# Optimization experiments

Measured on AMD Instinct MI355X. Metric: run time of the kernel, lower is better.

The kernel has to match this reference:

```python
import jax, jax.numpy as jnp
import numpy as np

B, L, H = 64, 512, 512          # batch, max_len, hidden_size (code requires H == L)
ITEM = 50001                    # item_num + 1
TEMP = 0.2                      # gumbel-sigmoid temperature
EPS = 1e-20


def setup_inputs() -> dict:
    key = jax.random.key(0)
    ks = jax.random.split(key, 16)
    lin = lambda k: jax.random.normal(k, (L, L), jnp.float32) * (1.0 / np.sqrt(L))
    U = jax.random.uniform(ks[13], (L, H), jnp.float32)
    gumbel = -jnp.log(-jnp.log(U + EPS) + EPS)
    return {
        "positives": jax.random.randint(ks[0], (B, L), 0, ITEM),
        "mask": jax.random.randint(ks[1], (B, L), 0, 2).astype(jnp.int32),
        "item_emb": jax.random.normal(ks[2], (ITEM, H), jnp.float32) * 0.02,
        "pos_emb": jax.random.normal(ks[3], (L, H), jnp.float32) * 0.02,
        "Wz": lin(ks[4]),
        "Wv": lin(ks[5]),
        "Wq": lin(ks[6]),
        "Wk": lin(ks[7]),
        "gamma_q": jax.random.normal(ks[8], (L,), jnp.float32) * 0.02,
        "beta_q": jnp.zeros((L,), jnp.float32),
        "gamma_k": jax.random.normal(ks[9], (L,), jnp.float32) * 0.02,
        "beta_k": jnp.zeros((L,), jnp.float32),
        "sparse_w": jax.random.uniform(ks[10], (L, H), jnp.float32, 0.2, 0.8),
        "gumbel": gumbel,
    }


def reference(positives, mask, item_emb, pos_emb, Wz, Wv, Wq, Wk,
              gamma_q, beta_q, gamma_k, beta_k, sparse_w, gumbel):
    # ---- merge_attn_masks: True = masked ----
    pad = ~(mask.astype(bool))[:, None, :]                 # [B,1,L]
    future = jnp.triu(jnp.ones((L, L), bool), k=1)         # strictly upper
    merged = pad | future[None]                            # [B,L,L]
    attn_mask = (~jnp.eye(L, dtype=bool))[None] & merged   # keep diagonal unmasked

    # ---- embeddings ----
    x = item_emb[positives] + pos_emb[None]                # [B,L,H]

    # ---- GAU-style projections (Linear acts on last dim, y = x @ W^T) ----
    z = jax.nn.silu(x @ Wz.T)                              # [B,L,H]
    v = jax.nn.silu(x @ Wv.T)                              # [B,L,H]
    q = (z @ Wq.T) * gamma_q + beta_q                      # OffsetScale head 0
    k = (z @ Wk.T) * gamma_k + beta_k

    # ---- relu^2 attention with bool mask added then zeroed ----
    m = attn_mask.astype(q.dtype)
    a = jnp.einsum('bld,bmd->blm', q, k) + m               # torch adds bool as 0/1
    a = a * (1.0 - m)                                      # a * ~attn_mask

    # ---- gumbel-sigmoid sparse mask (broadcast [L,L] over batch) ----
    smask = jax.nn.sigmoid((jnp.log(sparse_w / (1.0 - sparse_w)) + gumbel) / TEMP)
    a = smask[None] * a

    a = jnp.square(jax.nn.relu(a)) / (L * H)
    return a @ v                                           # [B,L,H]
```

## Files before the change

kernel.cpp:

```cpp
#include <hip/hip_runtime.h>
#include <hip/hip_fp16.h>
#include <math.h>

typedef _Float16 f16;
typedef unsigned int u32;
typedef _Float16 f16x8 __attribute__((ext_vector_type(8)));
typedef _Float16 f16x4 __attribute__((ext_vector_type(4)));
typedef float    f32x4 __attribute__((ext_vector_type(4)));

constexpr int LEN  = 512;
constexpr int HID  = 512;
constexpr int BATCH = 64;

#define BM 128
#define BN 128
#define BK 64

__device__ __forceinline__ void gload16(const f16* g, f16* l) {
    __builtin_amdgcn_global_load_lds((const __attribute__((address_space(1))) u32*)g,
                                     (__attribute__((address_space(3))) u32*)l,
                                     16, 0, 0);
}

__device__ __forceinline__ void gemm_core(const f16* __restrict__ A, int lda,
                                          const f16* __restrict__ Bm, int ldb,
                                          int ksteps,
                                          f16* ldsA, f16* ldsB,
                                          f32x4 acc[4][4])
{
    const int tid  = threadIdx.x;
    const int lane = tid & 63;
    const int wv   = tid >> 6;
    const int wr   = wv >> 1, wc = wv & 1;
    const int mf   = lane & 15;
    const int kf   = (lane >> 4) * 8;

    for (int r = 0; r < 4; ++r)
        for (int c = 0; c < 4; ++c)
            acc[r][c] = (f32x4){0.f, 0.f, 0.f, 0.f};

    for (int kt = 0; kt < ksteps; ++kt) {
        const int k0 = kt * BK;
        #pragma unroll
        for (int j = 0; j < 4; ++j) {
            const int cb  = j * 256 + wv * 64;
            const int c   = cb + lane;
            const int row = c >> 3;
            const int col = (c & 7) << 3;
            gload16(A  + (size_t)row * lda + (k0 + col), ldsA + cb * 8);
            gload16(Bm + (size_t)row * ldb + (k0 + col), ldsB + cb * 8);
        }
        __syncthreads();
        #pragma unroll
        for (int kk = 0; kk < BK; kk += 32) {
            f16x8 af[4], bf[4];
            #pragma unroll
            for (int r = 0; r < 4; ++r) {
                af[r] = *(const f16x8*)(ldsA + (wr * 64 + r * 16 + mf) * BK + kk + kf);
                bf[r] = *(const f16x8*)(ldsB + (wc * 64 + r * 16 + mf) * BK + kk + kf);
            }
            #pragma unroll
            for (int r = 0; r < 4; ++r)
                #pragma unroll
                for (int c = 0; c < 4; ++c)
                    acc[r][c] = __builtin_amdgcn_mfma_f32_16x16x32_f16(af[r], bf[c], acc[r][c], 0, 0, 0);
        }
        __syncthreads();
    }
}

#define EPILOGUE_IDX() \
    const int lane = threadIdx.x & 63, wv_ = threadIdx.x >> 6;   \
    const int wr = wv_ >> 1, wc = wv_ & 1;                       \
    const int c0 = lane & 15, r0 = (lane >> 4) * 4;

__device__ __forceinline__ void store_tile_f16(f16* lds, const f16 vals[4][4][4],
                                               f16* __restrict__ gout, int ldo)
{
    const int tid = threadIdx.x;
    EPILOGUE_IDX();
    #pragma unroll
    for (int r = 0; r < 4; ++r)
        #pragma unroll
        for (int c = 0; c < 4; ++c)
            #pragma unroll
            for (int i = 0; i < 4; ++i) {
                const int lr = wr * 64 + r * 16 + r0 + i;
                const int lc = wc * 64 + c * 16 + c0;
                lds[lr * 128 + lc] = vals[r][c][i];
            }
    __syncthreads();
    #pragma unroll
    for (int ph = 0; ph < 8; ++ph) {
        const int row = ph * 16 + (tid >> 4);
        const int col = (tid & 15) * 8;
        *(f16x8*)(gout + (size_t)row * ldo + col) = *(const f16x8*)(lds + row * 128 + col);
    }
}

__device__ __forceinline__ float silu_f(float v) {
    return v * __builtin_amdgcn_rcpf(1.f + __expf(-v));
}

__global__ __launch_bounds__(256) void k_zv(const f16* __restrict__ x,
                                            const f16* __restrict__ Wzh,
                                            const f16* __restrict__ Wvh,
                                            f16* __restrict__ z,
                                            f16* __restrict__ vt)
{
    const int bid = blockIdx.x;
    const int s = (bid & 7) + 8 * (bid >> 6);
    const int i = (bid >> 3) & 7;
    __shared__ f16 lds[(BM + BN) * BK];
    f32x4 acc[4][4];
    f16 vals[4][4][4];
    if (i < 4) {
        gemm_core(x + (size_t)s * BM * HID, HID,
                  Wzh + (size_t)i * BN * HID, HID,
                  HID / BK, lds, lds + BM * BK, acc);
        #pragma unroll
        for (int r = 0; r < 4; ++r)
            #pragma unroll
            for (int c = 0; c < 4; ++c)
                #pragma unroll
                for (int q = 0; q < 4; ++q)
                    vals[r][c][q] = (f16)silu_f(acc[r][c][q]);
        store_tile_f16(lds, vals, z + (size_t)s * BM * HID + i * BN, HID);
    } else {
        const int ht = i - 4, b = s >> 2, mt = s & 3;
        gemm_core(Wvh + (size_t)ht * BM * HID, HID,
                  x + ((size_t)b * LEN + mt * BN) * HID, HID,
                  HID / BK, lds, lds + BM * BK, acc);
        #pragma unroll
        for (int r = 0; r < 4; ++r)
            #pragma unroll
            for (int c = 0; c < 4; ++c)
                #pragma unroll
                for (int q = 0; q < 4; ++q)
                    vals[r][c][q] = (f16)silu_f(acc[r][c][q]);
        store_tile_f16(lds, vals,
                       vt + (size_t)b * LEN * HID + (size_t)ht * BM * LEN + mt * BN, LEN);
    }
}

__global__ __launch_bounds__(256) void k_qkp(const f16* __restrict__ z,
                                             const f16* __restrict__ Wqh,
                                             const f16* __restrict__ Wkh,
                                             const float* __restrict__ gq,
                                             const float* __restrict__ bq,
                                             const float* __restrict__ gk,
                                             const float* __restrict__ bk,
                                             f16* __restrict__ qh,
                                             f16* __restrict__ kh)
{
    const int bid = blockIdx.x;
    const int s = (bid & 7) + 8 * (bid >> 6);
    const int i = (bid >> 3) & 7;
    const bool isq = i < 4;
    const int tn = isq ? i : i - 4;
    const f16* W = isq ? Wqh : Wkh;
    const float* g = isq ? gq : gk;
    const float* be = isq ? bq : bk;
    f16* out = isq ? qh : kh;
    __shared__ f16 lds[(BM + BN) * BK];
    f32x4 acc[4][4];
    gemm_core(z + (size_t)s * BM * HID, HID,
              W + (size_t)tn * BN * HID, HID,
              HID / BK, lds, lds + BM * BK, acc);
    f16 vals[4][4][4];
    {
        EPILOGUE_IDX();
        #pragma unroll
        for (int r = 0; r < 4; ++r)
            #pragma unroll
            for (int c = 0; c < 4; ++c) {
                const int gj = tn * BN + wc * 64 + c * 16 + c0;
                const float ga = g[gj], ba = be[gj];
                #pragma unroll
                for (int q = 0; q < 4; ++q)
                    vals[r][c][q] = (f16)((acc[r][c][q] * ga + ba) * 1024.f);
            }
    }
    store_tile_f16(lds, vals, out + (size_t)s * BM * HID + tn * BN, HID);
}

__constant__ int LT_TAB[10] = {0,1,1,2,2,2,3,3,3,3};
__constant__ int MT_TAB[10] = {0,0,1,0,1,2,0,1,2,3};

__global__ __launch_bounds__(256) void k_qk(const f16* __restrict__ q,
                                            const f16* __restrict__ kmat,
                                            const int* __restrict__ mask,
                                            const float* __restrict__ smask,
                                            f16* __restrict__ p)
{
    const int bid = blockIdx.x;
    const int t = (bid >> 3) % 10;
    const int b = (bid & 7) + 8 * (bid / 80);
    const int lt = LT_TAB[t], mt = MT_TAB[t];
    __shared__ f16 lds[(BM + BN) * BK];
    f32x4 acc[4][4];
    const size_t boff = (size_t)b * LEN * HID;
    gemm_core(q + boff + (size_t)lt * BM * HID, HID,
              kmat + boff + (size_t)mt * BN * HID, HID,
              HID / BK, lds, lds + BM * BK, acc);
    f16 vals[4][4][4];
    {
        EPILOGUE_IDX();
        #pragma unroll
        for (int r = 0; r < 4; ++r)
            #pragma unroll
            for (int c = 0; c < 4; ++c) {
                const int m = mt * BN + wc * 64 + c * 16 + c0;
                const int keepcol = mask[b * LEN + m];
                #pragma unroll
                for (int i = 0; i < 4; ++i) {
                    const int l = lt * BM + wr * 64 + r * 16 + r0 + i;
                    const bool keep = (l == m) || ((m <= l) && (keepcol != 0));
                    float v = keep ? acc[r][c][i] * smask[l * LEN + m] : 0.f;
                    v = fmaxf(v, 0.f);
                    vals[r][c][i] = (f16)(v * v);
                }
            }
    }
    store_tile_f16(lds, vals, p + (size_t)b * LEN * LEN + (size_t)lt * BM * LEN + mt * BN, LEN);
}

__global__ __launch_bounds__(256) void k_pv(const f16* __restrict__ p,
                                            const f16* __restrict__ vt,
                                            float* __restrict__ out)
{
    const int bid = blockIdx.x;
    const int inner = (bid >> 3) & 15;
    const int b = (bid & 7) + 8 * (bid >> 7);
    const int lt = 3 - (inner >> 2), ht = inner & 3;
    __shared__ f16 lds[(BM + BN) * BK];
    f32x4 acc[4][4];
    gemm_core(p + (size_t)b * LEN * LEN + (size_t)lt * BM * LEN, LEN,
              vt + (size_t)b * HID * LEN + (size_t)ht * BN * LEN, LEN,
              (lt + 1) * BM / BK, lds, lds + BM * BK, acc);
    EPILOGUE_IDX();
    const float SCALE = 3.4694469519536142e-18f;
    #pragma unroll
    for (int r = 0; r < 4; ++r)
        #pragma unroll
        for (int c = 0; c < 4; ++c) {
            const int h = ht * BN + wc * 64 + c * 16 + c0;
            #pragma unroll
            for (int i = 0; i < 4; ++i) {
                const int l = lt * BM + wr * 64 + r * 16 + r0 + i;
                out[(size_t)b * LEN * HID + (size_t)l * HID + h] = acc[r][c][i] * SCALE;
            }
        }
}

__global__ __launch_bounds__(256) void k_prep(const int* __restrict__ pos,
                                              const float* __restrict__ item_emb,
                                              const float* __restrict__ pos_emb,
                                              f16* __restrict__ x,
                                              const float* __restrict__ Wz,
                                              const float* __restrict__ Wv,
                                              const float* __restrict__ Wq,
                                              const float* __restrict__ Wk,
                                              f16* __restrict__ Wzh,
                                              f16* __restrict__ Wvh,
                                              f16* __restrict__ Wqh,
                                              f16* __restrict__ Wkh,
                                              const float* __restrict__ sw,
                                              const float* __restrict__ gum,
                                              float* __restrict__ smask)
{
    const int bid = blockIdx.x;
    const int tid = threadIdx.x;
    if (bid < 16384) {
        const int t = bid * 256 + tid;
        const int i = t >> 7;
        const int c = t & 127;
        const int l = i & (LEN - 1);
        const int item = pos[i];
        const float4 a  = ((const float4*)(item_emb + (size_t)item * HID))[c];
        const float4 b4 = ((const float4*)(pos_emb + (size_t)l * HID))[c];
        f16x4 o = { (f16)(a.x + b4.x), (f16)(a.y + b4.y),
                    (f16)(a.z + b4.z), (f16)(a.w + b4.w) };
        *(f16x4*)(x + (size_t)t * 4) = o;
    } else if (bid < 16384 + 1024) {
        const int r = bid - 16384;
        const int w = r >> 8;
        const float* s = (w == 0) ? Wz : (w == 1) ? Wv : (w == 2) ? Wq : Wk;
        f16* d = (w == 0) ? Wzh : (w == 1) ? Wvh : (w == 2) ? Wqh : Wkh;
        const int t = (r & 255) * 256 + tid;
        const float4 v = ((const float4*)s)[t];
        f16x4 o = { (f16)v.x, (f16)v.y, (f16)v.z, (f16)v.w };
        *(f16x4*)(d + (size_t)t * 4) = o;
    } else {
        const int t = (bid - 16384 - 1024) * 256 + tid;
        const float4 w4 = ((const float4*)sw)[t];
        const float4 g4 = ((const float4*)gum)[t];
        float4 o;
        o.x = __builtin_amdgcn_rcpf(1.f + __expf(-(__logf(w4.x / (1.f - w4.x)) + g4.x) * 5.f));
        o.y = __builtin_amdgcn_rcpf(1.f + __expf(-(__logf(w4.y / (1.f - w4.y)) + g4.y) * 5.f));
        o.z = __builtin_amdgcn_rcpf(1.f + __expf(-(__logf(w4.z / (1.f - w4.z)) + g4.z) * 5.f));
        o.w = __builtin_amdgcn_rcpf(1.f + __expf(-(__logf(w4.w / (1.f - w4.w)) + g4.w) * 5.f));
        ((float4*)smask)[t] = o;
    }
}

extern "C" void kernel_launch(void* const* d_in, const int* in_sizes, int n_in,
                              void* d_out, int out_size, void* d_ws, size_t ws_size,
                              hipStream_t stream)
{
    const int*   positives = (const int*)  d_in[0];
    const int*   mask      = (const int*)  d_in[1];
    const float* item_emb  = (const float*)d_in[2];
    const float* pos_emb   = (const float*)d_in[3];
    const float* Wz        = (const float*)d_in[4];
    const float* Wv        = (const float*)d_in[5];
    const float* Wq        = (const float*)d_in[6];
    const float* Wk        = (const float*)d_in[7];
    const float* gamma_q   = (const float*)d_in[8];
    const float* beta_q    = (const float*)d_in[9];
    const float* gamma_k   = (const float*)d_in[10];
    const float* beta_k    = (const float*)d_in[11];
    const float* sparse_w  = (const float*)d_in[12];
    const float* gumbel    = (const float*)d_in[13];
    float* out = (float*)d_out;

    char* ws = (char*)d_ws;
    const size_t BUFB = (size_t)BATCH * LEN * HID * sizeof(f16);
    f16* buf0 = (f16*)ws;
    f16* buf1 = (f16*)(ws + BUFB);
    f16* buf2 = (f16*)(ws + 2 * BUFB);
    f16* Wzh  = (f16*)(ws + 3 * BUFB);
    f16* Wvh  = Wzh + LEN * HID;
    f16* Wqh  = Wvh + LEN * HID;
    f16* Wkh  = Wqh + LEN * HID;
    float* smask = (float*)(Wkh + LEN * HID);
    f16* qh = (f16*)d_out;
    f16* kh = qh + (size_t)BATCH * LEN * HID;

    k_prep<<<16384 + 1024 + 256, 256, 0, stream>>>(
        positives, item_emb, pos_emb, buf0,
        Wz, Wv, Wq, Wk, Wzh, Wvh, Wqh, Wkh,
        sparse_w, gumbel, smask);

    k_zv<<<2048, 256, 0, stream>>>(buf0, Wzh, Wvh, buf1, buf2);

    k_qkp<<<2048, 256, 0, stream>>>(buf1, Wqh, Wkh,
                                    gamma_q, beta_q, gamma_k, beta_k, qh, kh);

    k_qk<<<640, 256, 0, stream>>>(qh, kh, mask, smask, buf0);

    k_pv<<<1024, 256, 0, stream>>>(buf0, buf2, out);
}
```

Before: 372.6 us.

## Replace projection GEMMs with 256x256 tiled, triple-buffered 8-wave kernels

The z/v and q/k projection kernels move from 128x128 tiles with 256 threads to 256x256 tiles with 512 threads (8 waves). Each wave computes a 128x64 sub-tile. K is consumed in 32-wide steps through a three-deep LDS ring filled by direct global-to-LDS loads with XOR-swizzled slots, and MFMA bursts are interleaved with staged loads under raised wave priority. The aim is more operand reuse per byte loaded and better overlap of memory with compute. In exchange each block uses about 136 KB of LDS, and the grid shrinks to 512 blocks, which lowers occupancy.

```diff
diff --git a/kernel.cpp b/kernel.cpp
--- a/kernel.cpp
+++ b/kernel.cpp
@@ -20,6 +20,200 @@
     __builtin_amdgcn_global_load_lds((const __attribute__((address_space(1))) u32*)g,
                                      (__attribute__((address_space(3))) u32*)l,
                                      16, 0, 0);
+}
+
+__device__ __forceinline__ float silu_f(float v) {
+    return v * __builtin_amdgcn_rcpf(1.f + __expf(-v));
+}
+
+#define LDSP 272
+
+__device__ __forceinline__ void stage_pass8(const f16* __restrict__ g, f16* l) {
+    const int tid = threadIdx.x;
+    const int row = tid >> 2;
+    const int sc  = (tid & 3) ^ (row & 3);
+    gload16(g + (size_t)row * HID + sc * 8, l + (tid >> 6) * 512);
+}
+
+__device__ __forceinline__ void stage_tile8(const f16* __restrict__ A,
+                                            const f16* __restrict__ B,
+                                            int kt, f16* buf) {
+    stage_pass8(A + kt * 32,             buf);
+    stage_pass8(A + kt * 32 + 128 * HID, buf + 4096);
+    stage_pass8(B + kt * 32,             buf + 8192);
+    stage_pass8(B + kt * 32 + 128 * HID, buf + 12288);
+}
+
+__device__ __forceinline__ void gemm8_core(const f16* __restrict__ A,
+                                           const f16* __restrict__ B,
+                                           f16* lds, f32x4 acc[8][4])
+{
+    const int tid  = threadIdx.x;
+    const int lane = tid & 63;
+    const int wv   = tid >> 6;
+    const int wr   = wv >> 2, wc = wv & 3;
+    const int mf   = lane & 15;
+    const int slot = ((lane >> 4) ^ (mf & 3)) * 8;
+    const int aoff = (wr * 128 + mf) * 32 + slot;
+    const int boff = (wc * 64  + mf) * 32 + slot + 8192;
+
+    #pragma unroll
+    for (int m = 0; m < 8; ++m)
+        #pragma unroll
+        for (int n = 0; n < 4; ++n)
+            acc[m][n] = (f32x4){0.f, 0.f, 0.f, 0.f};
+
+    stage_tile8(A, B, 0, lds);
+    stage_tile8(A, B, 1, lds + 16384);
+    asm volatile("s_waitcnt vmcnt(4)" ::: "memory");
+    __builtin_amdgcn_s_barrier();
+
+    f16x8 af[4], bf[4];
+    #pragma unroll
+    for (int kt = 0; kt < 16; ++kt) {
+        f16* buf  = lds + (kt % 3) * 16384;
+        f16* nbuf = lds + ((kt + 2) % 3) * 16384;
+        const bool st = (kt < 14);
+
+        #pragma unroll
+        for (int m = 0; m < 4; ++m) af[m] = *(const f16x8*)(buf + aoff + m * 512);
+        #pragma unroll
+        for (int n = 0; n < 4; ++n) bf[n] = *(const f16x8*)(buf + boff + n * 512);
+        if (st) {
+            stage_pass8(A + (kt + 2) * 32,             nbuf);
+            stage_pass8(A + (kt + 2) * 32 + 128 * HID, nbuf + 4096);
+        }
+        __builtin_amdgcn_s_barrier();
+        asm volatile("s_waitcnt lgkmcnt(0)" ::: "memory");
+        __builtin_amdgcn_sched_barrier(0);
+        __builtin_amdgcn_s_setprio(1);
+        #pragma unroll
+        for (int m = 0; m < 4; ++m)
+            #pragma unroll
+            for (int n = 0; n < 4; ++n)
+                acc[m][n] = __builtin_amdgcn_mfma_f32_16x16x32_f16(af[m], bf[n], acc[m][n], 0, 0, 0);
+        __builtin_amdgcn_s_setprio(0);
+        __builtin_amdgcn_s_barrier();
+
+        #pragma unroll
+        for (int m = 0; m < 4; ++m) af[m] = *(const f16x8*)(buf + aoff + (m + 4) * 512);
+        if (st) {
+            stage_pass8(B + (kt + 2) * 32,             nbuf + 8192);
+            stage_pass8(B + (kt + 2) * 32 + 128 * HID, nbuf + 12288);
+        }
+        __builtin_amdgcn_s_barrier();
+        asm volatile("s_waitcnt lgkmcnt(0)" ::: "memory");
+        __builtin_amdgcn_sched_barrier(0);
+        __builtin_amdgcn_s_setprio(1);
+        #pragma unroll
+        for (int m = 0; m < 4; ++m)
+            #pragma unroll
+            for (int n = 0; n < 4; ++n)
+                acc[m + 4][n] = __builtin_amdgcn_mfma_f32_16x16x32_f16(af[m], bf[n], acc[m + 4][n], 0, 0, 0);
+        __builtin_amdgcn_s_setprio(0);
+        if (kt < 14)       asm volatile("s_waitcnt vmcnt(4)" ::: "memory");
+        else if (kt == 14) asm volatile("s_waitcnt vmcnt(0)" ::: "memory");
+        __builtin_amdgcn_s_barrier();
+    }
+}
+
+__device__ __forceinline__ void store_tile8(const f16* lds, f16* __restrict__ gout, int ldo) {
+    const int tid = threadIdx.x;
+    #pragma unroll
+    for (int ph = 0; ph < 16; ++ph) {
+        const int r = ph * 16 + (tid >> 5);
+        const int c = (tid & 31) * 8;
+        *(f16x8*)(gout + (size_t)r * ldo + c) = *(const f16x8*)(lds + r * LDSP + c);
+    }
+}
+
+#define EPI8_IDX() \
+    const int lane = threadIdx.x & 63, wv_ = threadIdx.x >> 6;  \
+    const int wr = wv_ >> 2, wc = wv_ & 3;                      \
+    const int c0 = lane & 15, r0 = (lane >> 4) * 4;
+
+__global__ __launch_bounds__(512, 2) void k_zv8(const f16* __restrict__ x,
+                                                const f16* __restrict__ Wzh,
+                                                const f16* __restrict__ Wvh,
+                                                f16* __restrict__ z,
+                                                f16* __restrict__ vt)
+{
+    __shared__ __align__(16) f16 lds[256 * LDSP];
+    const int bid = blockIdx.x;
+    const int s  = (bid & 7) + 8 * (bid >> 5);
+    const int ci = (bid >> 3) & 3;
+    const f16* A; const f16* Bm; f16* gout;
+    if (ci < 2) {
+        A = x + (size_t)s * 256 * HID;
+        Bm = Wzh + (size_t)ci * 256 * HID;
+        gout = z + (size_t)s * 256 * HID + ci * 256;
+    } else {
+        const int ht = ci - 2, b = s >> 1, mt = s & 1;
+        A = Wvh + (size_t)ht * 256 * HID;
+        Bm = x + ((size_t)b * LEN + mt * 256) * HID;
+        gout = vt + (size_t)b * HID * LEN + (size_t)ht * 256 * LEN + mt * 256;
+    }
+    f32x4 acc[8][4];
+    gemm8_core(A, Bm, lds, acc);
+    __syncthreads();
+    {
+        EPI8_IDX();
+        #pragma unroll
+        for (int m = 0; m < 8; ++m)
+            #pragma unroll
+            for (int n = 0; n < 4; ++n)
+                #pragma unroll
+                for (int i = 0; i < 4; ++i) {
+                    const int row = wr * 128 + m * 16 + r0 + i;
+                    const int col = wc * 64 + n * 16 + c0;
+                    lds[row * LDSP + col] = (f16)silu_f(acc[m][n][i]);
+                }
+    }
+    __syncthreads();
+    store_tile8(lds, gout, 512);
+}
+
+__global__ __launch_bounds__(512, 2) void k_qkp8(const f16* __restrict__ z,
+                                                 const f16* __restrict__ Wqh,
+                                                 const f16* __restrict__ Wkh,
+                                                 const float* __restrict__ gq,
+                                                 const float* __restrict__ bq,
+                                                 const float* __restrict__ gk,
+                                                 const float* __restrict__ bk,
+                                                 f16* __restrict__ qh,
+                                                 f16* __restrict__ kh)
+{
+    __shared__ __align__(16) f16 lds[256 * LDSP];
+    const int bid = blockIdx.x;
+    const int s  = (bid & 7) + 8 * (bid >> 5);
+    const int ci = (bid >> 3) & 3;
+    const bool isq = ci < 2;
+    const int nt = isq ? ci : ci - 2;
+    const f16* W = isq ? Wqh : Wkh;
+    const float* g  = isq ? gq : gk;
+    const float* be = isq ? bq : bk;
+    f16* outp = isq ? qh : kh;
+    f32x4 acc[8][4];
+    gemm8_core(z + (size_t)s * 256 * HID, W + (size_t)nt * 256 * HID, lds, acc);
+    __syncthreads();
+    {
+        EPI8_IDX();
+        #pragma unroll
+        for (int n = 0; n < 4; ++n) {
+            const int col = wc * 64 + n * 16 + c0;
+            const int jg = nt * 256 + col;
+            const float ga = g[jg], ba = be[jg];
+            #pragma unroll
+            for (int m = 0; m < 8; ++m)
+                #pragma unroll
+                for (int i = 0; i < 4; ++i) {
+                    const int row = wr * 128 + m * 16 + r0 + i;
+                    lds[row * LDSP + col] = (f16)((acc[m][n][i] * ga + ba) * 1024.f);
+                }
+        }
+    }
+    __syncthreads();
+    store_tile8(lds, outp + (size_t)s * 256 * HID + nt * 256, 512);
 }
 
 __device__ __forceinline__ void gemm_core(const f16* __restrict__ A, int lda,
@@ -96,92 +290,6 @@
         const int col = (tid & 15) * 8;
         *(f16x8*)(gout + (size_t)row * ldo + col) = *(const f16x8*)(lds + row * 128 + col);
     }
-}
-
-__device__ __forceinline__ float silu_f(float v) {
-    return v * __builtin_amdgcn_rcpf(1.f + __expf(-v));
-}
-
-__global__ __launch_bounds__(256) void k_zv(const f16* __restrict__ x,
-                                            const f16* __restrict__ Wzh,
-                                            const f16* __restrict__ Wvh,
-                                            f16* __restrict__ z,
-                                            f16* __restrict__ vt)
-{
-    const int bid = blockIdx.x;
-    const int s = (bid & 7) + 8 * (bid >> 6);
-    const int i = (bid >> 3) & 7;
-    __shared__ f16 lds[(BM + BN) * BK];
-    f32x4 acc[4][4];
-    f16 vals[4][4][4];
-    if (i < 4) {
-        gemm_core(x + (size_t)s * BM * HID, HID,
-                  Wzh + (size_t)i * BN * HID, HID,
-                  HID / BK, lds, lds + BM * BK, acc);
-        #pragma unroll
-        for (int r = 0; r < 4; ++r)
-            #pragma unroll
-            for (int c = 0; c < 4; ++c)
-                #pragma unroll
-                for (int q = 0; q < 4; ++q)
-                    vals[r][c][q] = (f16)silu_f(acc[r][c][q]);
-        store_tile_f16(lds, vals, z + (size_t)s * BM * HID + i * BN, HID);
-    } else {
-        const int ht = i - 4, b = s >> 2, mt = s & 3;
-        gemm_core(Wvh + (size_t)ht * BM * HID, HID,
-                  x + ((size_t)b * LEN + mt * BN) * HID, HID,
-                  HID / BK, lds, lds + BM * BK, acc);
-        #pragma unroll
-        for (int r = 0; r < 4; ++r)
-            #pragma unroll
-            for (int c = 0; c < 4; ++c)
-                #pragma unroll
-                for (int q = 0; q < 4; ++q)
-                    vals[r][c][q] = (f16)silu_f(acc[r][c][q]);
-        store_tile_f16(lds, vals,
-                       vt + (size_t)b * LEN * HID + (size_t)ht * BM * LEN + mt * BN, LEN);
-    }
-}
-
-__global__ __launch_bounds__(256) void k_qkp(const f16* __restrict__ z,
-                                             const f16* __restrict__ Wqh,
-                                             const f16* __restrict__ Wkh,
-                                             const float* __restrict__ gq,
-                                             const float* __restrict__ bq,
-                                             const float* __restrict__ gk,
-                                             const float* __restrict__ bk,
-                                             f16* __restrict__ qh,
-                                             f16* __restrict__ kh)
-{
-    const int bid = blockIdx.x;
-    const int s = (bid & 7) + 8 * (bid >> 6);
-    const int i = (bid >> 3) & 7;
-    const bool isq = i < 4;
-    const int tn = isq ? i : i - 4;
-    const f16* W = isq ? Wqh : Wkh;
-    const float* g = isq ? gq : gk;
-    const float* be = isq ? bq : bk;
-    f16* out = isq ? qh : kh;
-    __shared__ f16 lds[(BM + BN) * BK];
-    f32x4 acc[4][4];
-    gemm_core(z + (size_t)s * BM * HID, HID,
-              W + (size_t)tn * BN * HID, HID,
-              HID / BK, lds, lds + BM * BK, acc);
-    f16 vals[4][4][4];
-    {
-        EPILOGUE_IDX();
-        #pragma unroll
-        for (int r = 0; r < 4; ++r)
-            #pragma unroll
-            for (int c = 0; c < 4; ++c) {
-                const int gj = tn * BN + wc * 64 + c * 16 + c0;
-                const float ga = g[gj], ba = be[gj];
-                #pragma unroll
-                for (int q = 0; q < 4; ++q)
-                    vals[r][c][q] = (f16)((acc[r][c][q] * ga + ba) * 1024.f);
-            }
-    }
-    store_tile_f16(lds, vals, out + (size_t)s * BM * HID + tn * BN, HID);
 }
 
 __constant__ int LT_TAB[10] = {0,1,1,2,2,2,3,3,3,3};
@@ -342,9 +450,9 @@
         Wz, Wv, Wq, Wk, Wzh, Wvh, Wqh, Wkh,
         sparse_w, gumbel, smask);
 
-    k_zv<<<2048, 256, 0, stream>>>(buf0, Wzh, Wvh, buf1, buf2);
-
-    k_qkp<<<2048, 256, 0, stream>>>(buf1, Wqh, Wkh,
+    k_zv8<<<512, 512, 0, stream>>>(buf0, Wzh, Wvh, buf1, buf2);
+
+    k_qkp8<<<512, 512, 0, stream>>>(buf1, Wqh, Wkh,
                                     gamma_q, beta_q, gamma_k, beta_k, qh, kh);
 
     k_qk<<<640, 256, 0, stream>>>(qh, kh, mask, smask, buf0);
```

Measured after the change: 354.8 us. 4.8% less time.

## Switch GEMM kernels to 8-wave 256x128 tiles with triple-buffered swizzled LDS pipeline

Applied to the files above, without the earlier changes.

Replaces the single-buffered 4-wave 128x128 GEMM core with a 512-thread kernel that stages 256x128 tiles of BK=32 into a three-deep LDS ring. It uses XOR-swizzled layout, vmcnt-counted waits and s_setprio around the MFMA block. The goal is to overlap global-to-LDS loads with MFMA work and to cut bank conflicts and barrier stalls. The causal QK and PV grids are coarsened to 256-row tiles, which computes somewhat more masked work. Epilogues now stage output through padded LDS in two halves.

```diff
diff --git a/kernel.cpp b/kernel.cpp
--- a/kernel.cpp
+++ b/kernel.cpp
@@ -12,243 +12,271 @@
 constexpr int HID  = 512;
 constexpr int BATCH = 64;
 
-#define BM 128
-#define BN 128
-#define BK 64
-
 __device__ __forceinline__ void gload16(const f16* g, f16* l) {
     __builtin_amdgcn_global_load_lds((const __attribute__((address_space(1))) u32*)g,
                                      (__attribute__((address_space(3))) u32*)l,
                                      16, 0, 0);
 }
 
-__device__ __forceinline__ void gemm_core(const f16* __restrict__ A, int lda,
-                                          const f16* __restrict__ Bm, int ldb,
-                                          int ksteps,
-                                          f16* ldsA, f16* ldsB,
-                                          f32x4 acc[4][4])
-{
-    const int tid  = threadIdx.x;
-    const int lane = tid & 63;
-    const int wv   = tid >> 6;
-    const int wr   = wv >> 1, wc = wv & 1;
-    const int mf   = lane & 15;
-    const int kf   = (lane >> 4) * 8;
-
-    for (int r = 0; r < 4; ++r)
-        for (int c = 0; c < 4; ++c)
-            acc[r][c] = (f32x4){0.f, 0.f, 0.f, 0.f};
-
-    for (int kt = 0; kt < ksteps; ++kt) {
-        const int k0 = kt * BK;
-        #pragma unroll
-        for (int j = 0; j < 4; ++j) {
-            const int cb  = j * 256 + wv * 64;
-            const int c   = cb + lane;
-            const int row = c >> 3;
-            const int col = (c & 7) << 3;
-            gload16(A  + (size_t)row * lda + (k0 + col), ldsA + cb * 8);
-            gload16(Bm + (size_t)row * ldb + (k0 + col), ldsB + cb * 8);
-        }
-        __syncthreads();
-        #pragma unroll
-        for (int kk = 0; kk < BK; kk += 32) {
-            f16x8 af[4], bf[4];
-            #pragma unroll
-            for (int r = 0; r < 4; ++r) {
-                af[r] = *(const f16x8*)(ldsA + (wr * 64 + r * 16 + mf) * BK + kk + kf);
-                bf[r] = *(const f16x8*)(ldsB + (wc * 64 + r * 16 + mf) * BK + kk + kf);
-            }
-            #pragma unroll
-            for (int r = 0; r < 4; ++r)
-                #pragma unroll
-                for (int c = 0; c < 4; ++c)
-                    acc[r][c] = __builtin_amdgcn_mfma_f32_16x16x32_f16(af[r], bf[c], acc[r][c], 0, 0, 0);
-        }
-        __syncthreads();
-    }
-}
-
-#define EPILOGUE_IDX() \
-    const int lane = threadIdx.x & 63, wv_ = threadIdx.x >> 6;   \
-    const int wr = wv_ >> 1, wc = wv_ & 1;                       \
-    const int c0 = lane & 15, r0 = (lane >> 4) * 4;
-
-__device__ __forceinline__ void store_tile_f16(f16* lds, const f16 vals[4][4][4],
-                                               f16* __restrict__ gout, int ldo)
-{
-    const int tid = threadIdx.x;
-    EPILOGUE_IDX();
-    #pragma unroll
-    for (int r = 0; r < 4; ++r)
-        #pragma unroll
-        for (int c = 0; c < 4; ++c)
-            #pragma unroll
-            for (int i = 0; i < 4; ++i) {
-                const int lr = wr * 64 + r * 16 + r0 + i;
-                const int lc = wc * 64 + c * 16 + c0;
-                lds[lr * 128 + lc] = vals[r][c][i];
-            }
-    __syncthreads();
-    #pragma unroll
-    for (int ph = 0; ph < 8; ++ph) {
-        const int row = ph * 16 + (tid >> 4);
-        const int col = (tid & 15) * 8;
-        *(f16x8*)(gout + (size_t)row * ldo + col) = *(const f16x8*)(lds + row * 128 + col);
-    }
-}
-
 __device__ __forceinline__ float silu_f(float v) {
     return v * __builtin_amdgcn_rcpf(1.f + __expf(-v));
 }
 
-__global__ __launch_bounds__(256) void k_zv(const f16* __restrict__ x,
-                                            const f16* __restrict__ Wzh,
-                                            const f16* __restrict__ Wvh,
-                                            f16* __restrict__ z,
-                                            f16* __restrict__ vt)
-{
-    const int bid = blockIdx.x;
-    const int s = (bid & 7) + 8 * (bid >> 6);
-    const int i = (bid >> 3) & 7;
-    __shared__ f16 lds[(BM + BN) * BK];
+#define TUNIT 12288
+#define EPIP  136
+
+__device__ __forceinline__ void stage_pass(const f16* __restrict__ g, f16* l) {
+    const int tid = threadIdx.x;
+    const int row = tid >> 2;
+    const int sc  = (tid & 3) ^ ((row >> 1) & 3);
+    gload16(g + (size_t)row * 512 + sc * 8, l + (tid >> 6) * 512);
+}
+
+__device__ __forceinline__ void stage_tile(const f16* __restrict__ A,
+                                           const f16* __restrict__ B,
+                                           int kt, f16* buf) {
+    stage_pass(A + kt * 32,             buf);
+    stage_pass(A + kt * 32 + 128 * 512, buf + 4096);
+    stage_pass(B + kt * 32,             buf + 8192);
+}
+
+__device__ __forceinline__ void gemm8b(const f16* __restrict__ A,
+                                       const f16* __restrict__ B,
+                                       int ksteps, f16* lds, f32x4 acc[4][4])
+{
+    const int lane = threadIdx.x & 63;
+    const int wv   = threadIdx.x >> 6;
+    const int wr = wv >> 1, wc = wv & 1;
+    const int mf = lane & 15;
+    const int slot = ((lane >> 4) ^ ((mf >> 1) & 3)) * 8;
+    const int aoff = (wr * 64 + mf) * 32 + slot;
+    const int boff = (wc * 64 + mf) * 32 + slot + 8192;
+
+    #pragma unroll
+    for (int m = 0; m < 4; ++m)
+        #pragma unroll
+        for (int n = 0; n < 4; ++n)
+            acc[m][n] = (f32x4){0.f, 0.f, 0.f, 0.f};
+
+    stage_tile(A, B, 0, lds);
+    stage_tile(A, B, 1, lds + TUNIT);
+    asm volatile("s_waitcnt vmcnt(3)" ::: "memory");
+    __builtin_amdgcn_s_barrier();
+
+    int cb = 0;
+    for (int kt = 0; kt < ksteps; ++kt) {
+        f16* buf = lds + cb * TUNIT;
+        f16x8 af[4], bf[4];
+        #pragma unroll
+        for (int m = 0; m < 4; ++m) af[m] = *(const f16x8*)(buf + aoff + m * 512);
+        #pragma unroll
+        for (int n = 0; n < 4; ++n) bf[n] = *(const f16x8*)(buf + boff + n * 512);
+        if (kt + 2 < ksteps) {
+            int nb = cb + 2; if (nb >= 3) nb -= 3;
+            stage_tile(A, B, kt + 2, lds + nb * TUNIT);
+        }
+        asm volatile("s_waitcnt lgkmcnt(0)" ::: "memory");
+        __builtin_amdgcn_sched_barrier(0);
+        __builtin_amdgcn_s_setprio(1);
+        #pragma unroll
+        for (int m = 0; m < 4; ++m)
+            #pragma unroll
+            for (int n = 0; n < 4; ++n)
+                acc[m][n] = __builtin_amdgcn_mfma_f32_16x16x32_f16(af[m], bf[n], acc[m][n], 0, 0, 0);
+        __builtin_amdgcn_s_setprio(0);
+        if (kt + 3 <= ksteps) {
+            asm volatile("s_waitcnt vmcnt(3)" ::: "memory");
+            __builtin_amdgcn_s_barrier();
+        } else if (kt + 2 == ksteps) {
+            asm volatile("s_waitcnt vmcnt(0)" ::: "memory");
+            __builtin_amdgcn_s_barrier();
+        }
+        cb = cb + 1; if (cb >= 3) cb = 0;
+    }
+}
+
+#define EPI_IDX() \
+    const int lane = threadIdx.x & 63, wv_ = threadIdx.x >> 6;  \
+    const int wr = wv_ >> 1, wc = wv_ & 1;                      \
+    const int c0 = lane & 15, r0 = (lane >> 4) * 4;
+
+__device__ __forceinline__ void copy_half(const f16* lds, f16* __restrict__ gout,
+                                          int ldo, int h) {
+    const int tid = threadIdx.x;
+    #pragma unroll
+    for (int ph = 0; ph < 4; ++ph) {
+        const int r = ph * 32 + (tid >> 4);
+        const int c = (tid & 15) * 8;
+        *(f16x8*)(gout + (size_t)(h * 128 + r) * ldo + c) = *(const f16x8*)(lds + r * EPIP + c);
+    }
+}
+
+__global__ __launch_bounds__(512, 4) void k_zv8(const f16* __restrict__ x,
+                                                const f16* __restrict__ Wzh,
+                                                const f16* __restrict__ Wvh,
+                                                f16* __restrict__ z,
+                                                f16* __restrict__ vt)
+{
+    __shared__ __align__(16) f16 lds[3 * TUNIT];
+    const int bid = blockIdx.x;
+    const int s  = (bid & 7) + 8 * (bid >> 6);
+    const int ci = (bid >> 3) & 7;
+    const f16* A; const f16* Bm; f16* gout;
+    if (ci < 4) {
+        A = x + (size_t)s * 256 * HID;
+        Bm = Wzh + (size_t)ci * 128 * HID;
+        gout = z + (size_t)s * 256 * HID + ci * 128;
+    } else {
+        const int ht = (ci - 4) >> 1, lh = (ci - 4) & 1;
+        A = Wvh + (size_t)ht * 256 * HID;
+        Bm = x + ((size_t)s * 256 + lh * 128) * HID;
+        gout = vt + (size_t)(s >> 1) * LEN * HID + (size_t)ht * 256 * LEN
+                  + (s & 1) * 256 + lh * 128;
+    }
     f32x4 acc[4][4];
-    f16 vals[4][4][4];
-    if (i < 4) {
-        gemm_core(x + (size_t)s * BM * HID, HID,
-                  Wzh + (size_t)i * BN * HID, HID,
-                  HID / BK, lds, lds + BM * BK, acc);
-        #pragma unroll
-        for (int r = 0; r < 4; ++r)
-            #pragma unroll
-            for (int c = 0; c < 4; ++c)
+    gemm8b(A, Bm, HID / 32, lds, acc);
+    __syncthreads();
+    EPI_IDX();
+    #pragma unroll
+    for (int h = 0; h < 2; ++h) {
+        if ((wr >> 1) == h) {
+            const int rb = (wr & 1) * 64;
+            #pragma unroll
+            for (int m = 0; m < 4; ++m)
                 #pragma unroll
-                for (int q = 0; q < 4; ++q)
-                    vals[r][c][q] = (f16)silu_f(acc[r][c][q]);
-        store_tile_f16(lds, vals, z + (size_t)s * BM * HID + i * BN, HID);
-    } else {
-        const int ht = i - 4, b = s >> 2, mt = s & 3;
-        gemm_core(Wvh + (size_t)ht * BM * HID, HID,
-                  x + ((size_t)b * LEN + mt * BN) * HID, HID,
-                  HID / BK, lds, lds + BM * BK, acc);
-        #pragma unroll
-        for (int r = 0; r < 4; ++r)
-            #pragma unroll
-            for (int c = 0; c < 4; ++c)
+                for (int n = 0; n < 4; ++n)
+                    #pragma unroll
+                    for (int i = 0; i < 4; ++i)
+                        lds[(rb + m * 16 + r0 + i) * EPIP + wc * 64 + n * 16 + c0] =
+                            (f16)silu_f(acc[m][n][i]);
+        }
+        __syncthreads();
+        copy_half(lds, gout, 512, h);
+        __syncthreads();
+    }
+}
+
+__global__ __launch_bounds__(512, 4) void k_qkp8(const f16* __restrict__ z,
+                                                 const f16* __restrict__ Wqh,
+                                                 const f16* __restrict__ Wkh,
+                                                 const float* __restrict__ gq,
+                                                 const float* __restrict__ bq,
+                                                 const float* __restrict__ gk,
+                                                 const float* __restrict__ bk,
+                                                 f16* __restrict__ qh,
+                                                 f16* __restrict__ kh)
+{
+    __shared__ __align__(16) f16 lds[3 * TUNIT];
+    const int bid = blockIdx.x;
+    const int s  = (bid & 7) + 8 * (bid >> 6);
+    const int ci = (bid >> 3) & 7;
+    const bool isq = ci < 4;
+    const int nt = ci & 3;
+    const f16* W = isq ? Wqh : Wkh;
+    const float* g  = isq ? gq : gk;
+    const float* be = isq ? bq : bk;
+    f16* outp = isq ? qh : kh;
+    f32x4 acc[4][4];
+    gemm8b(z + (size_t)s * 256 * HID, W + (size_t)nt * 128 * HID, HID / 32, lds, acc);
+    __syncthreads();
+    EPI_IDX();
+    f16* gbase = outp + (size_t)s * 256 * HID + nt * 128;
+    #pragma unroll
+    for (int h = 0; h < 2; ++h) {
+        if ((wr >> 1) == h) {
+            const int rb = (wr & 1) * 64;
+            #pragma unroll
+            for (int n = 0; n < 4; ++n) {
+                const int col = wc * 64 + n * 16 + c0;
+                const int jg = nt * 128 + col;
+                const float ga = g[jg], ba = be[jg];
                 #pragma unroll
-                for (int q = 0; q < 4; ++q)
-                    vals[r][c][q] = (f16)silu_f(acc[r][c][q]);
-        store_tile_f16(lds, vals,
-                       vt + (size_t)b * LEN * HID + (size_t)ht * BM * LEN + mt * BN, LEN);
-    }
-}
-
-__global__ __launch_bounds__(256) void k_qkp(const f16* __restrict__ z,
-                                             const f16* __restrict__ Wqh,
-                                             const f16* __restrict__ Wkh,
-                                             const float* __restrict__ gq,
-                                             const float* __restrict__ bq,
-                                             const float* __restrict__ gk,
-                                             const float* __restrict__ bk,
-                                             f16* __restrict__ qh,
-                                             f16* __restrict__ kh)
-{
-    const int bid = blockIdx.x;
-    const int s = (bid & 7) + 8 * (bid >> 6);
-    const int i = (bid >> 3) & 7;
-    const bool isq = i < 4;
-    const int tn = isq ? i : i - 4;
-    const f16* W = isq ? Wqh : Wkh;
-    const float* g = isq ? gq : gk;
-    const float* be = isq ? bq : bk;
-    f16* out = isq ? qh : kh;
-    __shared__ f16 lds[(BM + BN) * BK];
+                for (int m = 0; m < 4; ++m)
+                    #pragma unroll
+                    for (int i = 0; i < 4; ++i)
+                        lds[(rb + m * 16 + r0 + i) * EPIP + col] =
+                            (f16)((acc[m][n][i] * ga + ba) * 1024.f);
+            }
+        }
+        __syncthreads();
+        copy_half(lds, gbase, 512, h);
+        __syncthreads();
+    }
+}
+
+__constant__ int LT6[6] = {0,0,1,1,1,1};
+__constant__ int MT6[6] = {0,1,0,1,2,3};
+
+__global__ __launch_bounds__(512, 4) void k_qk8(const f16* __restrict__ q,
+                                                const f16* __restrict__ kmat,
+                                                const int* __restrict__ mask,
+                                                const float* __restrict__ smask,
+                                                f16* __restrict__ p)
+{
+    __shared__ __align__(16) f16 lds[3 * TUNIT];
+    const int bid = blockIdx.x;
+    const int t = (bid >> 3) % 6;
+    const int b = (bid & 7) + 8 * (bid / 48);
+    const int lt = LT6[t], mt = MT6[t];
+    const size_t boff = (size_t)b * LEN * HID;
     f32x4 acc[4][4];
-    gemm_core(z + (size_t)s * BM * HID, HID,
-              W + (size_t)tn * BN * HID, HID,
-              HID / BK, lds, lds + BM * BK, acc);
-    f16 vals[4][4][4];
-    {
-        EPILOGUE_IDX();
-        #pragma unroll
-        for (int r = 0; r < 4; ++r)
-            #pragma unroll
-            for (int c = 0; c < 4; ++c) {
-                const int gj = tn * BN + wc * 64 + c * 16 + c0;
-                const float ga = g[gj], ba = be[gj];
+    gemm8b(q + boff + (size_t)lt * 256 * HID,
+           kmat + boff + (size_t)mt * 128 * HID, HID / 32, lds, acc);
+    __syncthreads();
+    EPI_IDX();
+    f16* gbase = p + (size_t)b * LEN * LEN + (size_t)lt * 256 * LEN + mt * 128;
+    #pragma unroll
+    for (int h = 0; h < 2; ++h) {
+        if ((wr >> 1) == h) {
+            const int rb = (wr & 1) * 64;
+            #pragma unroll
+            for (int n = 0; n < 4; ++n) {
+                const int col = wc * 64 + n * 16 + c0;
+                const int m_g = mt * 128 + col;
+                const int keepcol = mask[b * LEN + m_g];
                 #pragma unroll
-                for (int q = 0; q < 4; ++q)
-                    vals[r][c][q] = (f16)((acc[r][c][q] * ga + ba) * 1024.f);
+                for (int m = 0; m < 4; ++m)
+                    #pragma unroll
+                    for (int i = 0; i < 4; ++i) {
+                        const int row = rb + m * 16 + r0 + i;
+                        const int l_g = lt * 256 + h * 128 + row;
+                        const bool keep = (l_g == m_g) || ((m_g <= l_g) && (keepcol != 0));
+                        float v = keep ? acc[m][n][i] * smask[l_g * LEN + m_g] : 0.f;
+                        v = fmaxf(v, 0.f);
+                        lds[row * EPIP + col] = (f16)(v * v);
+                    }
             }
-    }
-    store_tile_f16(lds, vals, out + (size_t)s * BM * HID + tn * BN, HID);
-}
-
-__constant__ int LT_TAB[10] = {0,1,1,2,2,2,3,3,3,3};
-__constant__ int MT_TAB[10] = {0,0,1,0,1,2,0,1,2,3};
-
-__global__ __launch_bounds__(256) void k_qk(const f16* __restrict__ q,
-                                            const f16* __restrict__ kmat,
-                                            const int* __restrict__ mask,
-                                            const float* __restrict__ smask,
-                                            f16* __restrict__ p)
-{
-    const int bid = blockIdx.x;
-    const int t = (bid >> 3) % 10;
-    const int b = (bid & 7) + 8 * (bid / 80);
-    const int lt = LT_TAB[t], mt = MT_TAB[t];
-    __shared__ f16 lds[(BM + BN) * BK];
+        }
+        __syncthreads();
+        copy_half(lds, gbase, 512, h);
+        __syncthreads();
+    }
+}
+
+__global__ __launch_bounds__(512, 4) void k_pv8(const f16* __restrict__ p,
+                                                const f16* __restrict__ vt,
+                                                float* __restrict__ out)
+{
+    __shared__ __align__(16) f16 lds[3 * TUNIT];
+    const int bid = blockIdx.x;
+    const int inner = (bid >> 3) & 7;
+    const int b = (bid & 7) + 8 * (bid >> 6);
+    const int lt = 1 - (inner >> 2), ht = inner & 3;
     f32x4 acc[4][4];
-    const size_t boff = (size_t)b * LEN * HID;
-    gemm_core(q + boff + (size_t)lt * BM * HID, HID,
-              kmat + boff + (size_t)mt * BN * HID, HID,
-              HID / BK, lds, lds + BM * BK, acc);
-    f16 vals[4][4][4];
-    {
-        EPILOGUE_IDX();
-        #pragma unroll
-        for (int r = 0; r < 4; ++r)
-            #pragma unroll
-            for (int c = 0; c < 4; ++c) {
-                const int m = mt * BN + wc * 64 + c * 16 + c0;
-                const int keepcol = mask[b * LEN + m];
-                #pragma unroll
-                for (int i = 0; i < 4; ++i) {
-                    const int l = lt * BM + wr * 64 + r * 16 + r0 + i;
-                    const bool keep = (l == m) || ((m <= l) && (keepcol != 0));
-                    float v = keep ? acc[r][c][i] * smask[l * LEN + m] : 0.f;
-                    v = fmaxf(v, 0.f);
-                    vals[r][c][i] = (f16)(v * v);
-                }
-            }
-    }
-    store_tile_f16(lds, vals, p + (size_t)b * LEN * LEN + (size_t)lt * BM * LEN + mt * BN, LEN);
-}
-
-__global__ __launch_bounds__(256) void k_pv(const f16* __restrict__ p,
-                                            const f16* __restrict__ vt,
-                                            float* __restrict__ out)
-{
-    const int bid = blockIdx.x;
-    const int inner = (bid >> 3) & 15;
-    const int b = (bid & 7) + 8 * (bid >> 7);
-    const int lt = 3 - (inner >> 2), ht = inner & 3;
-    __shared__ f16 lds[(BM + BN) * BK];
-    f32x4 acc[4][4];
-    gemm_core(p + (size_t)b * LEN * LEN + (size_t)lt * BM * LEN, LEN,
-              vt + (size_t)b * HID * LEN + (size_t)ht * BN * LEN, LEN,
-              (lt + 1) * BM / BK, lds, lds + BM * BK, acc);
-    EPILOGUE_IDX();
+    gemm8b(p + (size_t)b * LEN * LEN + (size_t)lt * 256 * LEN,
+           vt + (size_t)b * HID * LEN + (size_t)ht * 128 * LEN,
+           (lt + 1) * 8, lds, acc);
+    EPI_IDX();
     const float SCALE = 3.4694469519536142e-18f;
     #pragma unroll
-    for (int r = 0; r < 4; ++r)
-        #pragma unroll
-        for (int c = 0; c < 4; ++c) {
-            const int h = ht * BN + wc * 64 + c * 16 + c0;
+    for (int m = 0; m < 4; ++m)
+        #pragma unroll
+        for (int n = 0; n < 4; ++n) {
+            const int h = ht * 128 + wc * 64 + n * 16 + c0;
             #pragma unroll
             for (int i = 0; i < 4; ++i) {
-                const int l = lt * BM + wr * 64 + r * 16 + r0 + i;
-                out[(size_t)b * LEN * HID + (size_t)l * HID + h] = acc[r][c][i] * SCALE;
+                const int l = lt * 256 + wr * 64 + m * 16 + r0 + i;
+                out[(size_t)b * LEN * HID + (size_t)l * HID + h] = acc[m][n][i] * SCALE;
             }
         }
 }
@@ -342,12 +370,12 @@
         Wz, Wv, Wq, Wk, Wzh, Wvh, Wqh, Wkh,
         sparse_w, gumbel, smask);
 
-    k_zv<<<2048, 256, 0, stream>>>(buf0, Wzh, Wvh, buf1, buf2);
-
-    k_qkp<<<2048, 256, 0, stream>>>(buf1, Wqh, Wkh,
-                                    gamma_q, beta_q, gamma_k, beta_k, qh, kh);
-
-    k_qk<<<640, 256, 0, stream>>>(qh, kh, mask, smask, buf0);
-
-    k_pv<<<1024, 256, 0, stream>>>(buf0, buf2, out);
-}
+    k_zv8<<<1024, 512, 0, stream>>>(buf0, Wzh, Wvh, buf1, buf2);
+
+    k_qkp8<<<1024, 512, 0, stream>>>(buf1, Wqh, Wkh,
+                                     gamma_q, beta_q, gamma_k, beta_k, qh, kh);
+
+    k_qk8<<<384, 512, 0, stream>>>(qh, kh, mask, smask, buf0);
+
+    k_pv8<<<512, 512, 0, stream>>>(buf0, buf2, out);
+}
```

Result: faster. 344.1 us (-7.7%).
